# Kernel tuning notes

Hardware: AMD Instinct MI355X
Metric: run time of the kernel (lower is better)

The kernel has to match this reference:

```python
import jax, jax.numpy as jnp
import numpy as np

B, T, C, H, FF = 4, 2048, 768, 12, 3072
D = C // H
EPS = 1e-5


def setup_inputs() -> dict:
    key = jax.random.key(0)
    ks = jax.random.split(key, 8)
    s = 0.02
    return {
        "x": jax.random.normal(ks[0], (B, T, C), jnp.float32),
        "ln1_w": jnp.ones((C,), jnp.float32),
        "ln1_b": jnp.zeros((C,), jnp.float32),
        "qkv_w": jax.random.normal(ks[1], (C, 3 * C), jnp.float32) * s,
        "qkv_b": jnp.zeros((3 * C,), jnp.float32),
        "out_w": jax.random.normal(ks[2], (C, C), jnp.float32) * s,
        "out_b": jnp.zeros((C,), jnp.float32),
        "ln2_w": jnp.ones((C,), jnp.float32),
        "ln2_b": jnp.zeros((C,), jnp.float32),
        "ff1_w": jax.random.normal(ks[3], (C, FF), jnp.float32) * s,
        "ff1_b": jnp.zeros((FF,), jnp.float32),
        "ff2_w": jax.random.normal(ks[4], (FF, C), jnp.float32) * s,
        "ff2_b": jnp.zeros((C,), jnp.float32),
    }


def _layernorm(x, w, b):
    m = jnp.mean(x, axis=-1, keepdims=True)
    v = jnp.mean(jnp.square(x - m), axis=-1, keepdims=True)
    return (x - m) * jax.lax.rsqrt(v + EPS) * w + b


def reference(x, ln1_w, ln1_b, qkv_w, qkv_b, out_w, out_b,
              ln2_w, ln2_b, ff1_w, ff1_b, ff2_w, ff2_b):
    # --- attention sublayer ---
    h = _layernorm(x, ln1_w, ln1_b)
    qkv = h @ qkv_w + qkv_b                      # [B,T,3C]
    q, k, v = jnp.split(qkv, 3, axis=-1)
    q = q.reshape(B, T, H, D)
    k = k.reshape(B, T, H, D)
    v = v.reshape(B, T, H, D)
    scores = jnp.einsum('bthd,bshd->bhts', q, k) / np.sqrt(D).astype(np.float32)
    causal = jnp.tril(jnp.ones((T, T), bool))    # [T,T]
    scores = jnp.where(causal[None, None], scores, -jnp.inf)
    attn = jax.nn.softmax(scores, axis=-1)       # [B,H,T,T]
    o = jnp.einsum('bhts,bshd->bthd', attn, v).reshape(B, T, C)
    x = x + o @ out_w + out_b
    # --- FFN sublayer ---
    h2 = _layernorm(x, ln2_w, ln2_b)
    x = x + jax.nn.relu(h2 @ ff1_w + ff1_b) @ ff2_w + ff2_b
    return x
```

## Files before the change

### kernel.cpp

```cpp
#include <hip/hip_runtime.h>
#include <hip/hip_bf16.h>
#include <cstdint>
#include <cstddef>

#define B_ 4
#define T_ 2048
#define C_ 768
#define H_ 12
#define D_ 64
#define FF_ 3072

typedef __attribute__((ext_vector_type(4))) float f32x4;
typedef __attribute__((ext_vector_type(8))) short s16x8;
typedef __attribute__((ext_vector_type(4))) short s16x4;

static __device__ __forceinline__ short f2bf(float f) {
  union { float fv; unsigned u; } v; v.fv = f;
  unsigned r = v.u + 0x7FFFu + ((v.u >> 16) & 1u);
  return (short)(r >> 16);
}

static __device__ __forceinline__ unsigned pkbf2(float a, float b) {
  __hip_bfloat162 h = __float22bfloat162_rn(make_float2(a, b));
  union { __hip_bfloat162 h2; unsigned u; } v; v.h2 = h;
  return v.u;
}

__global__ __launch_bounds__(256) void wconv(const float* __restrict__ in,
                                             short* __restrict__ out,
                                             int K, int N) {
  __shared__ float tile[32][33];
  int tk = blockIdx.x * 32, tn = blockIdx.y * 32;
  int lx = threadIdx.x & 31, ly = threadIdx.x >> 5;
#pragma unroll
  for (int i = 0; i < 4; ++i)
    tile[ly + i * 8][lx] = in[(size_t)(tk + ly + i * 8) * N + tn + lx];
  __syncthreads();
#pragma unroll
  for (int i = 0; i < 4; ++i)
    out[(size_t)(tn + ly + i * 8) * K + tk + lx] = f2bf(tile[lx][ly + i * 8]);
}

__global__ __launch_bounds__(256) void ln_kernel(const float* __restrict__ x,
                                                 const float* __restrict__ w,
                                                 const float* __restrict__ b,
                                                 short* __restrict__ out) {
  int row = blockIdx.x, tid = threadIdx.x;
  const float* xr = x + (size_t)row * 768;
  float v0 = xr[tid], v1 = xr[tid + 256], v2 = xr[tid + 512];
  float s = v0 + v1 + v2;
#pragma unroll
  for (int o = 32; o > 0; o >>= 1) s += __shfl_down(s, o);
  __shared__ float r1[4], r2[4];
  if ((tid & 63) == 0) r1[tid >> 6] = s;
  __syncthreads();
  float mean = (r1[0] + r1[1] + r1[2] + r1[3]) * (1.f / 768.f);
  float d0 = v0 - mean, d1 = v1 - mean, d2 = v2 - mean;
  float q = d0 * d0 + d1 * d1 + d2 * d2;
#pragma unroll
  for (int o = 32; o > 0; o >>= 1) q += __shfl_down(q, o);
  if ((tid & 63) == 0) r2[tid >> 6] = q;
  __syncthreads();
  float var = (r2[0] + r2[1] + r2[2] + r2[3]) * (1.f / 768.f);
  float rstd = rsqrtf(var + 1e-5f);
  short* orow = out + (size_t)row * 768;
  orow[tid]       = f2bf(d0 * rstd * w[tid]       + b[tid]);
  orow[tid + 256] = f2bf(d1 * rstd * w[tid + 256] + b[tid + 256]);
  orow[tid + 512] = f2bf(d2 * rstd * w[tid + 512] + b[tid + 512]);
}

template <int MODE>
__global__ __launch_bounds__(256) void gemm_bt(
    const short* __restrict__ A, const short* __restrict__ Bt,
    const float* __restrict__ bias, const float* __restrict__ res,
    void* __restrict__ out,
    short* __restrict__ dq, short* __restrict__ dk, short* __restrict__ dv,
    int M, int N, int K) {
  __shared__ short As[2][128 * 32];
  __shared__ short Bs[2][128 * 32];
  int tid = threadIdx.x;
  int lane = tid & 63;
  int wm = tid >> 7;
  int wn = (tid >> 6) & 1;
  const short* Ab = A + (size_t)blockIdx.x * 128 * K;
  const short* Bb = Bt + (size_t)blockIdx.y * 128 * K;
  f32x4 acc[4][4] = {};
  int i15 = lane & 15, g8 = (lane >> 4) << 3;
  int nk = K >> 6;
  for (int kt = 0; kt < nk; ++kt) {
    int kof = kt << 6;
#pragma unroll
    for (int i = 0; i < 4; ++i) {
      int s = tid + i * 256;
      int pan = s >> 9, sp = s & 511;
      int row = sp >> 2, kk = ((sp & 3) << 3) + (pan << 5);
      __builtin_amdgcn_global_load_lds(
          (const __attribute__((address_space(1))) unsigned*)(Ab + (size_t)row * K + kof + kk),
          (__attribute__((address_space(3))) unsigned*)(&As[pan][sp * 8]), 16, 0, 0);
      __builtin_amdgcn_global_load_lds(
          (const __attribute__((address_space(1))) unsigned*)(Bb + (size_t)row * K + kof + kk),
          (__attribute__((address_space(3))) unsigned*)(&Bs[pan][sp * 8]), 16, 0, 0);
    }
    __syncthreads();
#pragma unroll
    for (int h = 0; h < 2; ++h) {
      s16x8 af[4], bfr[4];
#pragma unroll
      for (int m = 0; m < 4; ++m)
        af[m] = *(const s16x8*)(&As[h][(wm * 64 + m * 16 + i15) * 32 + g8]);
#pragma unroll
      for (int n = 0; n < 4; ++n)
        bfr[n] = *(const s16x8*)(&Bs[h][(wn * 64 + n * 16 + i15) * 32 + g8]);
#pragma unroll
      for (int m = 0; m < 4; ++m)
#pragma unroll
        for (int n = 0; n < 4; ++n)
          acc[m][n] = __builtin_amdgcn_mfma_f32_16x16x32_bf16(af[m], bfr[n], acc[m][n], 0, 0, 0);
    }
    __syncthreads();
  }
  int row0 = blockIdx.x * 128 + wm * 64;
  int col0 = blockIdx.y * 128 + wn * 64;
  int g4 = (lane >> 4) << 2;
#pragma unroll
  for (int m = 0; m < 4; ++m) {
#pragma unroll
    for (int n = 0; n < 4; ++n) {
      int col = col0 + n * 16 + i15;
      float bv = bias[col];
      float v4[4];
#pragma unroll
      for (int r = 0; r < 4; ++r) v4[r] = acc[m][n][r] + bv;
      int rbase = row0 + m * 16 + g4;
      if constexpr (MODE == 0) {
        int sect = col / 768;
        int wi = col - sect * 768;
        int hh = wi >> 6, dd = wi & 63;
        int bb = rbase >> 11, tt = rbase & 2047;
        if (sect == 2) {
          s16x4 o4;
#pragma unroll
          for (int r = 0; r < 4; ++r) o4[r] = f2bf(v4[r]);
          *(s16x4*)(dv + ((size_t)(bb * H_ + hh) * D_ + dd) * T_ + tt) = o4;
        } else {
          short* dst = (sect == 0 ? dq : dk) + ((size_t)(bb * H_ + hh) * T_ + tt) * D_ + dd;
          float sc = sect == 0 ? 0.18033688f : 1.f;
#pragma unroll
          for (int r = 0; r < 4; ++r) dst[(size_t)r * D_] = f2bf(v4[r] * sc);
        }
      } else {
#pragma unroll
        for (int r = 0; r < 4; ++r)
          ((short*)out)[(size_t)(rbase + r) * N + col] = f2bf(v4[r] > 0.f ? v4[r] : 0.f);
      }
    }
  }
}

__global__ __launch_bounds__(128, 3) void gemm64_res(
    const short* __restrict__ A, const short* __restrict__ Bt,
    const float* __restrict__ bias, const float* __restrict__ res,
    float* __restrict__ out, int M, int N, int K) {
  __shared__ short As[2][64 * 32];
  __shared__ short Bs[2][128 * 32];
  int tid = threadIdx.x;
  int lane = tid & 63;
  int wn = tid >> 6;
  const short* Ab = A + (size_t)blockIdx.x * 64 * K;
  const short* Bb = Bt + (size_t)blockIdx.y * 128 * K;
  f32x4 acc[4][4] = {};
  int i15 = lane & 15, g8 = (lane >> 4) << 3;
  int nk = K >> 6;
  for (int kt = 0; kt < nk; ++kt) {
    int kof = kt << 6;
#pragma unroll
    for (int i = 0; i < 4; ++i) {
      int c = tid + i * 128;
      int pan = c >> 8, sp = c & 255;
      int row = sp >> 2, kk = ((sp & 3) << 3) + (pan << 5);
      __builtin_amdgcn_global_load_lds(
          (const __attribute__((address_space(1))) unsigned*)(Ab + (size_t)row * K + kof + kk),
          (__attribute__((address_space(3))) unsigned*)(&As[pan][sp * 8]), 16, 0, 0);
    }
#pragma unroll
    for (int i = 0; i < 8; ++i) {
      int c = tid + i * 128;
      int pan = c >> 9, sp = c & 511;
      int row = sp >> 2, kk = ((sp & 3) << 3) + (pan << 5);
      __builtin_amdgcn_global_load_lds(
          (const __attribute__((address_space(1))) unsigned*)(Bb + (size_t)row * K + kof + kk),
          (__attribute__((address_space(3))) unsigned*)(&Bs[pan][sp * 8]), 16, 0, 0);
    }
    __syncthreads();
#pragma unroll
    for (int h = 0; h < 2; ++h) {
      s16x8 af[4], bfr[4];
#pragma unroll
      for (int m = 0; m < 4; ++m)
        af[m] = *(const s16x8*)(&As[h][(m * 16 + i15) * 32 + g8]);
#pragma unroll
      for (int n = 0; n < 4; ++n)
        bfr[n] = *(const s16x8*)(&Bs[h][(wn * 64 + n * 16 + i15) * 32 + g8]);
#pragma unroll
      for (int m = 0; m < 4; ++m)
#pragma unroll
        for (int n = 0; n < 4; ++n)
          acc[m][n] = __builtin_amdgcn_mfma_f32_16x16x32_bf16(af[m], bfr[n], acc[m][n], 0, 0, 0);
    }
    __syncthreads();
  }
  int row0 = blockIdx.x * 64;
  int col0 = blockIdx.y * 128 + wn * 64;
  int g4 = (lane >> 4) << 2;
#pragma unroll
  for (int m = 0; m < 4; ++m) {
#pragma unroll
    for (int n = 0; n < 4; ++n) {
      int col = col0 + n * 16 + i15;
      float bv = bias[col];
      int rbase = row0 + m * 16 + g4;
#pragma unroll
      for (int r = 0; r < 4; ++r)
        out[(size_t)(rbase + r) * N + col] =
            acc[m][n][r] + bv + res[(size_t)(rbase + r) * N + col];
    }
  }
}

__global__ __launch_bounds__(256) void attn_kernel(const short* __restrict__ Qb,
                                                   const short* __restrict__ Kb,
                                                   const short* __restrict__ VTb,
                                                   short* __restrict__ Ob) {
  __shared__ short Ks[2][4096];
  __shared__ short Vs[2][4096];
  int i = blockIdx.x;
  int c = i & 7, j = i >> 3;
  int p = j & 15, gy = j >> 4;
  int bh = c + (gy << 3);
  int bb = bh / H_, hh = bh - bb * H_;
  int tid = threadIdx.x, lane = tid & 63, wv = tid >> 6;
  const short* Qp = Qb + (size_t)bh * T_ * D_;
  const short* Kp = Kb + (size_t)bh * T_ * D_;
  const short* Vp = VTb + (size_t)bh * D_ * T_;
  int i15 = lane & 15, g = lane >> 4, g8 = g << 3;
  int keyA0 = ((i15 >> 2) << 3) + (i15 & 3);
  int keyB0 = keyA0 + 4;
  int fA = (keyA0 & 7) ^ ((keyA0 & 8) >> 1);
  int fB = (keyB0 & 7) ^ ((keyB0 & 8) >> 1);
  int fV = (i15 & 7) ^ ((i15 & 8) >> 1);
  int oA[2], oB[2], oV[2];
#pragma unroll
  for (int h = 0; h < 2; ++h) {
    oA[h] = keyA0 * 64 + (((h * 4 + g) ^ fA) << 3);
    oB[h] = keyB0 * 64 + (((h * 4 + g) ^ fB) << 3);
    oV[h] = i15 * 64 + (((h * 4 + g) ^ fV) << 3);
  }
  int n0 = p + 1;
  s16x8 qf0, qf1;
  f32x4 oacc[4] = {};
  float lsum = 0.f;
  int qrow = 0;

  auto loadQ = [&](int qb) {
    qrow = (qb << 6) + wv * 16 + i15;
    qf0 = *(const s16x8*)(Qp + (size_t)qrow * D_ + g8);
    qf1 = *(const s16x8*)(Qp + (size_t)qrow * D_ + 32 + g8);
  };
  auto stage = [&](int buf, int t) {
    int k0 = t << 6;
#pragma unroll
    for (int qq = 0; qq < 2; ++qq) {
      int m = tid + qq * 256;
      int r = m >> 3, cd = m & 7;
      int cs = cd ^ ((r & 7) ^ ((r & 8) >> 1));
      __builtin_amdgcn_global_load_lds(
          (const __attribute__((address_space(1))) unsigned*)(Kp + (size_t)(k0 + r) * D_ + (cs << 3)),
          (__attribute__((address_space(3))) unsigned*)(&Ks[buf][m * 8]), 16, 0, 0);
      __builtin_amdgcn_global_load_lds(
          (const __attribute__((address_space(1))) unsigned*)(Vp + (size_t)r * T_ + k0 + (cs << 3)),
          (__attribute__((address_space(3))) unsigned*)(&Vs[buf][m * 8]), 16, 0, 0);
    }
  };
  auto finalize = [&]() {
    float l = lsum;
    l += __shfl_xor(l, 16);
    l += __shfl_xor(l, 32);
    float inv = 1.f / l;
    short* op = Ob + ((size_t)(bb * T_ + qrow)) * C_ + hh * D_ + (g << 2);
#pragma unroll
    for (int mt = 0; mt < 4; ++mt) {
      s16x4 o4;
#pragma unroll
      for (int r = 0; r < 4; ++r) o4[r] = f2bf(oacc[mt][r] * inv);
      *(s16x4*)(op + mt * 16) = o4;
    }
  };

  loadQ(p);
  stage(0, 0);
  __syncthreads();
  int cur = 0;
#pragma unroll 1
  for (int gt = 0; gt < 33; ++gt) {
    if (gt + 1 < 33) {
      int nkt = (gt + 1 < n0) ? (gt + 1) : (gt + 1 - n0);
      stage(cur ^ 1, nkt);
    }
    int kt = (gt < n0) ? gt : gt - n0;
    int nt = (gt < n0) ? n0 : 32 - p;
    bool diag = (kt == nt - 1);
    int k0 = kt << 6;
    const short* KB = &Ks[cur][0];
    const short* VB = &Vs[cur][0];
#pragma unroll
    for (int ks = 0; ks < 2; ++ks) {
      if (!(ks == 1 && diag && wv < 2)) {
        s16x8 ka0 = *(const s16x8*)(KB + (ks << 11) + oA[0]);
        s16x8 ka1 = *(const s16x8*)(KB + (ks << 11) + oA[1]);
        s16x8 kb0 = *(const s16x8*)(KB + (ks << 11) + oB[0]);
        s16x8 kb1 = *(const s16x8*)(KB + (ks << 11) + oB[1]);
        f32x4 sA = {}, sB = {};
        __builtin_amdgcn_s_setprio(1);
        sA = __builtin_amdgcn_mfma_f32_16x16x32_bf16(ka0, qf0, sA, 0, 0, 0);
        sA = __builtin_amdgcn_mfma_f32_16x16x32_bf16(ka1, qf1, sA, 0, 0, 0);
        sB = __builtin_amdgcn_mfma_f32_16x16x32_bf16(kb0, qf0, sB, 0, 0, 0);
        sB = __builtin_amdgcn_mfma_f32_16x16x32_bf16(kb1, qf1, sB, 0, 0, 0);
        __builtin_amdgcn_s_setprio(0);
        int kb = k0 + (ks << 5) + g8;
        float sa[8];
        bool needmask = diag && ((wv < 2) == (ks == 0));
        if (needmask) {
#pragma unroll
          for (int r = 0; r < 4; ++r) {
            sa[r]     = (kb + r     <= qrow) ? sA[r] : -1e30f;
            sa[4 + r] = (kb + 4 + r <= qrow) ? sB[r] : -1e30f;
          }
        } else {
#pragma unroll
          for (int r = 0; r < 4; ++r) { sa[r] = sA[r]; sa[4 + r] = sB[r]; }
        }
        float pv[8];
        float ps = 0.f;
#pragma unroll
        for (int r = 0; r < 8; ++r) {
          pv[r] = exp2f(sa[r]);
          ps += pv[r];
        }
        lsum += ps;
        union { unsigned u[4]; s16x8 v; } pf;
        pf.u[0] = pkbf2(pv[0], pv[1]);
        pf.u[1] = pkbf2(pv[2], pv[3]);
        pf.u[2] = pkbf2(pv[4], pv[5]);
        pf.u[3] = pkbf2(pv[6], pv[7]);
        s16x8 vf0 = *(const s16x8*)(VB + 0    + oV[ks]);
        s16x8 vf1 = *(const s16x8*)(VB + 1024 + oV[ks]);
        s16x8 vf2 = *(const s16x8*)(VB + 2048 + oV[ks]);
        s16x8 vf3 = *(const s16x8*)(VB + 3072 + oV[ks]);
        __builtin_amdgcn_s_setprio(1);
        oacc[0] = __builtin_amdgcn_mfma_f32_16x16x32_bf16(vf0, pf.v, oacc[0], 0, 0, 0);
        oacc[1] = __builtin_amdgcn_mfma_f32_16x16x32_bf16(vf1, pf.v, oacc[1], 0, 0, 0);
        oacc[2] = __builtin_amdgcn_mfma_f32_16x16x32_bf16(vf2, pf.v, oacc[2], 0, 0, 0);
        oacc[3] = __builtin_amdgcn_mfma_f32_16x16x32_bf16(vf3, pf.v, oacc[3], 0, 0, 0);
        __builtin_amdgcn_s_setprio(0);
      }
    }
    if (gt == n0 - 1) {
      finalize();
      loadQ(31 - p);
#pragma unroll
      for (int mt = 0; mt < 4; ++mt) oacc[mt] = f32x4{0.f, 0.f, 0.f, 0.f};
      lsum = 0.f;
    }
    __syncthreads();
    cur ^= 1;
  }
  finalize();
}

extern "C" void kernel_launch(void* const* d_in, const int* in_sizes, int n_in,
                              void* d_out, int out_size, void* d_ws, size_t ws_size,
                              hipStream_t stream) {
  const float* x     = (const float*)d_in[0];
  const float* ln1_w = (const float*)d_in[1];
  const float* ln1_b = (const float*)d_in[2];
  const float* qkv_w = (const float*)d_in[3];
  const float* qkv_b = (const float*)d_in[4];
  const float* out_w = (const float*)d_in[5];
  const float* out_b = (const float*)d_in[6];
  const float* ln2_w = (const float*)d_in[7];
  const float* ln2_b = (const float*)d_in[8];
  const float* ff1_w = (const float*)d_in[9];
  const float* ff1_b = (const float*)d_in[10];
  const float* ff2_w = (const float*)d_in[11];
  const float* ff2_b = (const float*)d_in[12];

  char* ws = (char*)d_ws;
  short* Wqkv = (short*)(ws + 0);
  short* Wout = (short*)(ws + 3538944);
  short* Wff1 = (short*)(ws + 4718592);
  short* Wff2 = (short*)(ws + 9437184);
  short* Hbuf = (short*)(ws + 14155776);
  short* Qb   = (short*)(ws + 26738688);
  short* Kb   = Qb + 6291456;
  short* VT   = Kb + 6291456;
  short* Ob   = VT + 6291456;
  short* FFH  = Qb;
  float* xout = (float*)d_out;

  wconv<<<dim3(24, 72), 256, 0, stream>>>(qkv_w, Wqkv, 768, 2304);
  wconv<<<dim3(24, 24), 256, 0, stream>>>(out_w, Wout, 768, 768);
  wconv<<<dim3(24, 96), 256, 0, stream>>>(ff1_w, Wff1, 768, 3072);
  wconv<<<dim3(96, 24), 256, 0, stream>>>(ff2_w, Wff2, 3072, 768);

  ln_kernel<<<8192, 256, 0, stream>>>(x, ln1_w, ln1_b, Hbuf);
  gemm_bt<0><<<dim3(64, 18), 256, 0, stream>>>(Hbuf, Wqkv, qkv_b, nullptr, nullptr,
                                               Qb, Kb, VT, 8192, 2304, 768);
  attn_kernel<<<768, 256, 0, stream>>>(Qb, Kb, VT, Ob);
  gemm64_res<<<dim3(128, 6), 128, 0, stream>>>(Ob, Wout, out_b, x, xout, 8192, 768, 768);
  ln_kernel<<<8192, 256, 0, stream>>>(xout, ln2_w, ln2_b, Hbuf);
  gemm_bt<2><<<dim3(64, 24), 256, 0, stream>>>(Hbuf, Wff1, ff1_b, nullptr, FFH,
                                               nullptr, nullptr, nullptr, 8192, 3072, 768);
  gemm64_res<<<dim3(128, 6), 128, 0, stream>>>(FFH, Wff2, ff2_b, xout, xout, 8192, 768, 3072);
}
```

Measured before the change: 280.4 us.

## Double-buffer GEMM K-tiles with async LDS prefetch two stages ahead

Both bf16 GEMM kernels change from loading a full 64-wide K tile into two LDS panels and then computing, with no overlap, to a two-stage pipeline over 32-wide K tiles. The tile for step kt+2 is issued while step kt is computed, and the wait uses an explicit vmcnt so that only the oldest stage must land before the barrier. MFMA priority is raised with setprio and sched_barriers stop the compiler from reordering across the stage boundaries. This aims to hide global-load latency behind MFMA work, at the cost of twice as many loop iterations and barriers and a hand-tuned vmcnt that must match the number of loads issued per stage.

```diff
diff --git a/kernel.cpp b/kernel.cpp
--- a/kernel.cpp
+++ b/kernel.cpp
@@ -86,38 +86,50 @@
   const short* Bb = Bt + (size_t)blockIdx.y * 128 * K;
   f32x4 acc[4][4] = {};
   int i15 = lane & 15, g8 = (lane >> 4) << 3;
-  int nk = K >> 6;
+  int nk = K >> 5;
+  int r0 = tid >> 2, kc = (tid & 3) << 3;
+
+  auto stage = [&](int buf, int kt) {
+    int kof = kt << 5;
+    __builtin_amdgcn_global_load_lds(
+        (const __attribute__((address_space(1))) unsigned*)(Ab + (size_t)r0 * K + kof + kc),
+        (__attribute__((address_space(3))) unsigned*)(&As[buf][tid * 8]), 16, 0, 0);
+    __builtin_amdgcn_global_load_lds(
+        (const __attribute__((address_space(1))) unsigned*)(Bb + (size_t)r0 * K + kof + kc),
+        (__attribute__((address_space(3))) unsigned*)(&Bs[buf][tid * 8]), 16, 0, 0);
+    __builtin_amdgcn_global_load_lds(
+        (const __attribute__((address_space(1))) unsigned*)(Ab + (size_t)(r0 + 64) * K + kof + kc),
+        (__attribute__((address_space(3))) unsigned*)(&As[buf][(tid + 256) * 8]), 16, 0, 0);
+    __builtin_amdgcn_global_load_lds(
+        (const __attribute__((address_space(1))) unsigned*)(Bb + (size_t)(r0 + 64) * K + kof + kc),
+        (__attribute__((address_space(3))) unsigned*)(&Bs[buf][(tid + 256) * 8]), 16, 0, 0);
+  };
+
+  stage(0, 0);
+  stage(1, 1);
+  int cur = 0;
   for (int kt = 0; kt < nk; ++kt) {
-    int kof = kt << 6;
-#pragma unroll
-    for (int i = 0; i < 4; ++i) {
-      int s = tid + i * 256;
-      int pan = s >> 9, sp = s & 511;
-      int row = sp >> 2, kk = ((sp & 3) << 3) + (pan << 5);
-      __builtin_amdgcn_global_load_lds(
-          (const __attribute__((address_space(1))) unsigned*)(Ab + (size_t)row * K + kof + kk),
-          (__attribute__((address_space(3))) unsigned*)(&As[pan][sp * 8]), 16, 0, 0);
-      __builtin_amdgcn_global_load_lds(
-          (const __attribute__((address_space(1))) unsigned*)(Bb + (size_t)row * K + kof + kk),
-          (__attribute__((address_space(3))) unsigned*)(&Bs[pan][sp * 8]), 16, 0, 0);
-    }
-    __syncthreads();
-#pragma unroll
-    for (int h = 0; h < 2; ++h) {
-      s16x8 af[4], bfr[4];
-#pragma unroll
-      for (int m = 0; m < 4; ++m)
-        af[m] = *(const s16x8*)(&As[h][(wm * 64 + m * 16 + i15) * 32 + g8]);
+    asm volatile("s_waitcnt vmcnt(4)" ::: "memory");
+    __builtin_amdgcn_s_barrier();
+    __builtin_amdgcn_sched_barrier(0);
+    s16x8 af[4], bfr[4];
+#pragma unroll
+    for (int m = 0; m < 4; ++m)
+      af[m] = *(const s16x8*)(&As[cur][(wm * 64 + m * 16 + i15) * 32 + g8]);
+#pragma unroll
+    for (int n = 0; n < 4; ++n)
+      bfr[n] = *(const s16x8*)(&Bs[cur][(wn * 64 + n * 16 + i15) * 32 + g8]);
+    __builtin_amdgcn_s_setprio(1);
+#pragma unroll
+    for (int m = 0; m < 4; ++m)
 #pragma unroll
       for (int n = 0; n < 4; ++n)
-        bfr[n] = *(const s16x8*)(&Bs[h][(wn * 64 + n * 16 + i15) * 32 + g8]);
-#pragma unroll
-      for (int m = 0; m < 4; ++m)
-#pragma unroll
-        for (int n = 0; n < 4; ++n)
-          acc[m][n] = __builtin_amdgcn_mfma_f32_16x16x32_bf16(af[m], bfr[n], acc[m][n], 0, 0, 0);
-    }
-    __syncthreads();
+        acc[m][n] = __builtin_amdgcn_mfma_f32_16x16x32_bf16(af[m], bfr[n], acc[m][n], 0, 0, 0);
+    __builtin_amdgcn_s_setprio(0);
+    __builtin_amdgcn_sched_barrier(0);
+    __builtin_amdgcn_s_barrier();
+    if (kt + 2 < nk) stage(cur, kt + 2);
+    cur ^= 1;
   }
   int row0 = blockIdx.x * 128 + wm * 64;
   int col0 = blockIdx.y * 128 + wn * 64;
@@ -170,44 +182,53 @@
   const short* Bb = Bt + (size_t)blockIdx.y * 128 * K;
   f32x4 acc[4][4] = {};
   int i15 = lane & 15, g8 = (lane >> 4) << 3;
-  int nk = K >> 6;
-  for (int kt = 0; kt < nk; ++kt) {
-    int kof = kt << 6;
+  int nk = K >> 5;
+
+  auto stage = [&](int buf, int kt) {
+    int kof = kt << 5;
+#pragma unroll
+    for (int i = 0; i < 2; ++i) {
+      int c = tid + i * 128;
+      int row = c >> 2, kk = (c & 3) << 3;
+      __builtin_amdgcn_global_load_lds(
+          (const __attribute__((address_space(1))) unsigned*)(Ab + (size_t)row * K + kof + kk),
+          (__attribute__((address_space(3))) unsigned*)(&As[buf][c * 8]), 16, 0, 0);
+    }
 #pragma unroll
     for (int i = 0; i < 4; ++i) {
       int c = tid + i * 128;
-      int pan = c >> 8, sp = c & 255;
-      int row = sp >> 2, kk = ((sp & 3) << 3) + (pan << 5);
-      __builtin_amdgcn_global_load_lds(
-          (const __attribute__((address_space(1))) unsigned*)(Ab + (size_t)row * K + kof + kk),
-          (__attribute__((address_space(3))) unsigned*)(&As[pan][sp * 8]), 16, 0, 0);
-    }
-#pragma unroll
-    for (int i = 0; i < 8; ++i) {
-      int c = tid + i * 128;
-      int pan = c >> 9, sp = c & 511;
-      int row = sp >> 2, kk = ((sp & 3) << 3) + (pan << 5);
+      int row = c >> 2, kk = (c & 3) << 3;
       __builtin_amdgcn_global_load_lds(
           (const __attribute__((address_space(1))) unsigned*)(Bb + (size_t)row * K + kof + kk),
-          (__attribute__((address_space(3))) unsigned*)(&Bs[pan][sp * 8]), 16, 0, 0);
-    }
-    __syncthreads();
-#pragma unroll
-    for (int h = 0; h < 2; ++h) {
-      s16x8 af[4], bfr[4];
-#pragma unroll
-      for (int m = 0; m < 4; ++m)
-        af[m] = *(const s16x8*)(&As[h][(m * 16 + i15) * 32 + g8]);
+          (__attribute__((address_space(3))) unsigned*)(&Bs[buf][c * 8]), 16, 0, 0);
+    }
+  };
+
+  stage(0, 0);
+  stage(1, 1);
+  int cur = 0;
+  for (int kt = 0; kt < nk; ++kt) {
+    asm volatile("s_waitcnt vmcnt(6)" ::: "memory");
+    __builtin_amdgcn_s_barrier();
+    __builtin_amdgcn_sched_barrier(0);
+    s16x8 af[4], bfr[4];
+#pragma unroll
+    for (int m = 0; m < 4; ++m)
+      af[m] = *(const s16x8*)(&As[cur][(m * 16 + i15) * 32 + g8]);
+#pragma unroll
+    for (int n = 0; n < 4; ++n)
+      bfr[n] = *(const s16x8*)(&Bs[cur][(wn * 64 + n * 16 + i15) * 32 + g8]);
+    __builtin_amdgcn_s_setprio(1);
+#pragma unroll
+    for (int m = 0; m < 4; ++m)
 #pragma unroll
       for (int n = 0; n < 4; ++n)
-        bfr[n] = *(const s16x8*)(&Bs[h][(wn * 64 + n * 16 + i15) * 32 + g8]);
-#pragma unroll
-      for (int m = 0; m < 4; ++m)
-#pragma unroll
-        for (int n = 0; n < 4; ++n)
-          acc[m][n] = __builtin_amdgcn_mfma_f32_16x16x32_bf16(af[m], bfr[n], acc[m][n], 0, 0, 0);
-    }
-    __syncthreads();
+        acc[m][n] = __builtin_amdgcn_mfma_f32_16x16x32_bf16(af[m], bfr[n], acc[m][n], 0, 0, 0);
+    __builtin_amdgcn_s_setprio(0);
+    __builtin_amdgcn_sched_barrier(0);
+    __builtin_amdgcn_s_barrier();
+    if (kt + 2 < nk) stage(cur, kt + 2);
+    cur ^= 1;
   }
   int row0 = blockIdx.x * 64;
   int col0 = blockIdx.y * 128 + wn * 64;
```

Result: no change. 284.7 us (+1.5%).
